# Optimization experiments

Measured on AMD Instinct MI355X. Metric: run time of the kernel, lower is better.

## Reference

```python
import jax, jax.numpy as jnp
import numpy as np

N_LAYERS = 3

def setup_inputs() -> dict:
    key = jax.random.key(0)
    ks = jax.random.split(key, 16)
    N, E, F_in, H = 50000, 800000, 5, 64
    x = jax.random.normal(ks[0], (N, F_in), dtype=jnp.float32)
    edge_index = jax.random.randint(ks[1], (2, E), 0, N, dtype=jnp.int64)
    s = lambda fan_in: 1.0 / np.sqrt(fan_in)
    return {
        "x": x,
        "edge_index": edge_index,
        "W_enc": jax.random.uniform(ks[2], (F_in, H), jnp.float32, -s(F_in), s(F_in)),
        "b_enc": jnp.zeros((H,), jnp.float32),
        "conv_W": jax.random.uniform(ks[3], (N_LAYERS, H, H), jnp.float32, -s(H), s(H)),
        "conv_b": jnp.zeros((N_LAYERS, H), jnp.float32),
        "W_d1": jax.random.uniform(ks[4], (H, H // 2), jnp.float32, -s(H), s(H)),
        "b_d1": jnp.zeros((H // 2,), jnp.float32),
        "W_d2": jax.random.uniform(ks[5], (H // 2, 1), jnp.float32, -s(H // 2), s(H // 2)),
        "b_d2": jnp.zeros((1,), jnp.float32),
        "W_i1": jax.random.uniform(ks[6], (H, H // 2), jnp.float32, -s(H), s(H)),
        "b_i1": jnp.zeros((H // 2,), jnp.float32),
        "W_i2": jax.random.uniform(ks[7], (H // 2, 1), jnp.float32, -s(H // 2), s(H // 2)),
        "b_i2": jnp.zeros((1,), jnp.float32),
    }

def reference(x, edge_index, W_enc, b_enc, conv_W, conv_b,
              W_d1, b_d1, W_d2, b_d2, W_i1, b_i1, W_i2, b_i2):
    N = x.shape[0]
    # GCN normalization with self-loops (PyG GCNConv default):
    loops = jnp.arange(N, dtype=edge_index.dtype)
    row = jnp.concatenate([edge_index[0], loops])  # source
    col = jnp.concatenate([edge_index[1], loops])  # target
    deg = jax.ops.segment_sum(jnp.ones_like(row, dtype=x.dtype), col, num_segments=N)
    dinv = jax.lax.rsqrt(deg)  # deg >= 1 due to self-loops
    norm = dinv[row] * dinv[col]  # [E + N]

    h = jax.nn.relu(x @ W_enc + b_enc)  # [N, H]
    for l in range(N_LAYERS):
        hw = h @ conv_W[l]                       # [N, H]
        msg = hw[row] * norm[:, None]            # gather + scale
        agg = jax.ops.segment_sum(msg, col, num_segments=N)  # scatter-add
        h = jax.nn.relu(agg + conv_b[l])

    demand = jax.nn.relu(h @ W_d1 + b_d1) @ W_d2 + b_d2       # [N, 1]
    inventory = jax.nn.relu(h @ W_i1 + b_i1) @ W_i2 + b_i2    # [N, 1]
    return (demand, inventory)
```

## Files before the change

kernel.cpp:

```cpp
#include <hip/hip_runtime.h>
#include <hip/hip_bf16.h>


#define HDIM 64
#define PB 128
#define NPB 256
#define NPB_SHIFT 8

__device__ inline unsigned bfpack(float lo, float hi) {
    unsigned ul = __float_as_uint(lo), uh = __float_as_uint(hi);
    ul += 0x7fffu + ((ul >> 16) & 1u);
    uh += 0x7fffu + ((uh >> 16) & 1u);
    return (ul >> 16) | (uh & 0xffff0000u);
}

__device__ inline float2 bfunpack(unsigned u) {
    float2 r;
    r.x = __uint_as_float(u << 16);
    r.y = __uint_as_float(u & 0xffff0000u);
    return r;
}

__global__ __launch_bounds__(256) void hist_pass(const int* __restrict__ dst,
                                                 unsigned* __restrict__ histT,
                                                 int E, int NB) {
    __shared__ unsigned h[256];
    int t = threadIdx.x, p = blockIdx.x;
    h[t] = 0u;
    __syncthreads();
    int chunk = (E + PB - 1) / PB;
    int lo = p * chunk, hi = min(lo + chunk, E);
    for (int e = lo + t; e < hi; e += 256)
        atomicAdd(&h[dst[e] >> NPB_SHIFT], 1u);
    __syncthreads();
    if (t < NB) histT[t * PB + p] = h[t];
}

__global__ __launch_bounds__(128) void scan_bucket(unsigned* __restrict__ histT,
                                                   unsigned* __restrict__ btot) {
    __shared__ unsigned s[PB];
    int t = threadIdx.x, k = blockIdx.x;
    unsigned v = histT[k * PB + t];
    s[t] = v;
    __syncthreads();
#pragma unroll
    for (int off = 1; off < PB; off <<= 1) {
        unsigned u = (t >= off) ? s[t - off] : 0u;
        __syncthreads();
        s[t] += u;
        __syncthreads();
    }
    histT[k * PB + t] = s[t] - v;
    if (t == PB - 1) btot[k] = s[t];
}

__global__ __launch_bounds__(256) void bin_pass(const int* __restrict__ ei,
                                                const unsigned* __restrict__ histT,
                                                const unsigned* __restrict__ btot,
                                                unsigned* __restrict__ ebuf,
                                                int E, int NB) {
    __shared__ unsigned bb[256];
    __shared__ unsigned cur[256];
    int t = threadIdx.x, p = blockIdx.x;
    unsigned bv = (t < NB) ? btot[t] : 0u;
    bb[t] = bv;
    __syncthreads();
#pragma unroll
    for (int off = 1; off < 256; off <<= 1) {
        unsigned u = (t >= off) ? bb[t - off] : 0u;
        __syncthreads();
        bb[t] += u;
        __syncthreads();
    }
    if (t < NB) cur[t] = histT[t * PB + p] + (bb[t] - bv);
    __syncthreads();
    int chunk = (E + PB - 1) / PB;
    int lo = p * chunk, hi = min(lo + chunk, E);
    for (int e = lo + t; e < hi; e += 256) {
        unsigned sN = (unsigned)ei[e];
        unsigned dN = (unsigned)ei[E + e];
        unsigned pos = atomicAdd(&cur[dN >> NPB_SHIFT], 1u);
        ebuf[pos] = ((dN & (NPB - 1u)) << 16) | sN;
    }
}

__global__ __launch_bounds__(256) void csr_pass(const unsigned* __restrict__ ebuf,
                                                const unsigned* __restrict__ btot,
                                                unsigned* __restrict__ row_ptr,
                                                float* __restrict__ dinv,
                                                int* __restrict__ csr_src,
                                                int N, int E, int NB) {
    __shared__ unsigned bb[256];
    __shared__ unsigned cntL[NPB];
    __shared__ unsigned sc[NPB];
    __shared__ unsigned cur[NPB];
    int t = threadIdx.x, k = blockIdx.x;
    unsigned bv = (t < NB) ? btot[t] : 0u;
    bb[t] = bv;
    __syncthreads();
#pragma unroll
    for (int off = 1; off < 256; off <<= 1) {
        unsigned u = (t >= off) ? bb[t - off] : 0u;
        __syncthreads();
        bb[t] += u;
        __syncthreads();
    }
    unsigned e1 = bb[k];
    unsigned e0 = e1 - btot[k];
    int nbase = k << NPB_SHIFT;
    cntL[t] = 0u;
    __syncthreads();
    for (unsigned e = e0 + t; e < e1; e += 256)
        atomicAdd(&cntL[ebuf[e] >> 16], 1u);
    __syncthreads();
    unsigned v = cntL[t];
    sc[t] = v;
    __syncthreads();
#pragma unroll
    for (int off = 1; off < NPB; off <<= 1) {
        unsigned u = (t >= off) ? sc[t - off] : 0u;
        __syncthreads();
        sc[t] += u;
        __syncthreads();
    }
    unsigned pos0 = e0 + sc[t] - v;
    cur[t] = pos0;
    int node = nbase + t;
    if (node < N) {
        row_ptr[node] = pos0;
        dinv[node] = rsqrtf((float)(v + 1u));
    }
    if (k == NB - 1 && t == 0) row_ptr[N] = (unsigned)E;
    __syncthreads();
    for (unsigned e = e0 + t; e < e1; e += 256) {
        unsigned ed = ebuf[e];
        unsigned pos = atomicAdd(&cur[ed >> 16], 1u);
        csr_src[pos] = (int)(ed & 0xffffu);
    }
}

__global__ __launch_bounds__(256) void encoder(const float* __restrict__ x,
                                               const float* __restrict__ W,
                                               const float* __restrict__ b,
                                               const float* __restrict__ dinv,
                                               unsigned* __restrict__ hn, int N) {
    int t = blockIdx.x * 256 + threadIdx.x;
    int i = t >> 5, jp = t & 31;
    if (i >= N) return;
    int j0 = 2 * jp;
    float a0 = b[j0], a1 = b[j0 + 1];
#pragma unroll
    for (int k = 0; k < 5; k++) {
        float xv = x[i * 5 + k];
        a0 = fmaf(xv, W[k * 64 + j0], a0);
        a1 = fmaf(xv, W[k * 64 + j0 + 1], a1);
    }
    float di = dinv[i];
    hn[t] = bfpack(di * fmaxf(a0, 0.0f), di * fmaxf(a1, 0.0f));
}

__global__ __launch_bounds__(256, 6) void gather4(const unsigned int* __restrict__ row_ptr,
                                                  const int* __restrict__ csr_src,
                                                  const unsigned* __restrict__ hn,
                                                  float* __restrict__ g, int N) {
    int t = blockIdx.x * 256 + threadIdx.x;
    int i = t >> 5;
    if (i >= N) return;
    int fl = t & 31;
    float2 a0 = bfunpack(hn[(size_t)i * 32 + fl]);
    float2 a1 = {0.f, 0.f}, a2 = {0.f, 0.f}, a3 = {0.f, 0.f};
    float2 a4 = {0.f, 0.f}, a5 = {0.f, 0.f}, a6 = {0.f, 0.f}, a7 = {0.f, 0.f};
    unsigned e0 = row_ptr[i];
    unsigned cnt = row_ptr[i + 1] - e0;
    const int* idx = csr_src + e0;
    unsigned u = 0;
    if (cnt >= 8) {
        int s0 = idx[0], s1 = idx[1], s2 = idx[2], s3 = idx[3];
        int s4 = idx[4], s5 = idx[5], s6 = idx[6], s7 = idx[7];
        while (true) {
            unsigned v0 = hn[(size_t)s0 * 32 + fl];
            unsigned v1 = hn[(size_t)s1 * 32 + fl];
            unsigned v2 = hn[(size_t)s2 * 32 + fl];
            unsigned v3 = hn[(size_t)s3 * 32 + fl];
            unsigned v4 = hn[(size_t)s4 * 32 + fl];
            unsigned v5 = hn[(size_t)s5 * 32 + fl];
            unsigned v6 = hn[(size_t)s6 * 32 + fl];
            unsigned v7 = hn[(size_t)s7 * 32 + fl];
            unsigned un = u + 8;
            bool more = (un + 8 <= cnt);
            if (more) {
                s0 = idx[un + 0]; s1 = idx[un + 1]; s2 = idx[un + 2]; s3 = idx[un + 3];
                s4 = idx[un + 4]; s5 = idx[un + 5]; s6 = idx[un + 6]; s7 = idx[un + 7];
            }
            float2 f0 = bfunpack(v0), f1 = bfunpack(v1), f2 = bfunpack(v2), f3 = bfunpack(v3);
            float2 f4 = bfunpack(v4), f5 = bfunpack(v5), f6 = bfunpack(v6), f7 = bfunpack(v7);
            a0.x += f0.x; a0.y += f0.y;  a1.x += f1.x; a1.y += f1.y;
            a2.x += f2.x; a2.y += f2.y;  a3.x += f3.x; a3.y += f3.y;
            a4.x += f4.x; a4.y += f4.y;  a5.x += f5.x; a5.y += f5.y;
            a6.x += f6.x; a6.y += f6.y;  a7.x += f7.x; a7.y += f7.y;
            u = un;
            if (!more) break;
        }
    }
    if (u < cnt) {
        unsigned last = cnt - 1;
        int s0 = idx[u];
        int s1 = idx[min(u + 1, last)];
        int s2 = idx[min(u + 2, last)];
        int s3 = idx[min(u + 3, last)];
        int s4 = idx[min(u + 4, last)];
        int s5 = idx[min(u + 5, last)];
        int s6 = idx[min(u + 6, last)];
        int s7 = idx[min(u + 7, last)];
        unsigned v0 = hn[(size_t)s0 * 32 + fl];
        unsigned v1 = hn[(size_t)s1 * 32 + fl];
        unsigned v2 = hn[(size_t)s2 * 32 + fl];
        unsigned v3 = hn[(size_t)s3 * 32 + fl];
        unsigned v4 = hn[(size_t)s4 * 32 + fl];
        unsigned v5 = hn[(size_t)s5 * 32 + fl];
        unsigned v6 = hn[(size_t)s6 * 32 + fl];
        unsigned v7 = hn[(size_t)s7 * 32 + fl];
        float2 f0 = bfunpack(v0), f1 = bfunpack(v1), f2 = bfunpack(v2), f3 = bfunpack(v3);
        float2 f4 = bfunpack(v4), f5 = bfunpack(v5), f6 = bfunpack(v6), f7 = bfunpack(v7);
        a0.x += f0.x;                        a0.y += f0.y;
        a1.x += (u + 1 < cnt) ? f1.x : 0.f;  a1.y += (u + 1 < cnt) ? f1.y : 0.f;
        a2.x += (u + 2 < cnt) ? f2.x : 0.f;  a2.y += (u + 2 < cnt) ? f2.y : 0.f;
        a3.x += (u + 3 < cnt) ? f3.x : 0.f;  a3.y += (u + 3 < cnt) ? f3.y : 0.f;
        a4.x += (u + 4 < cnt) ? f4.x : 0.f;  a4.y += (u + 4 < cnt) ? f4.y : 0.f;
        a5.x += (u + 5 < cnt) ? f5.x : 0.f;  a5.y += (u + 5 < cnt) ? f5.y : 0.f;
        a6.x += (u + 6 < cnt) ? f6.x : 0.f;  a6.y += (u + 6 < cnt) ? f6.y : 0.f;
        a7.x += (u + 7 < cnt) ? f7.x : 0.f;  a7.y += (u + 7 < cnt) ? f7.y : 0.f;
    }
    a0.x += a1.x; a0.y += a1.y;  a2.x += a3.x; a2.y += a3.y;
    a4.x += a5.x; a4.y += a5.y;  a6.x += a7.x; a6.y += a7.y;
    a0.x += a2.x; a0.y += a2.y;  a4.x += a6.x; a4.y += a6.y;
    a0.x += a4.x; a0.y += a4.y;
    float2* g2 = (float2*)g;
    g2[(size_t)i * 32 + fl] = a0;
}

__global__ __launch_bounds__(256) void conv_relu(const float* __restrict__ g,
                                                 const float* __restrict__ W,
                                                 const float* __restrict__ b,
                                                 const float* __restrict__ dinv,
                                                 unsigned* __restrict__ houtB,
                                                 int N) {
    __shared__ float WT[64 * 68];
    int tid = threadIdx.x;
    for (int e = tid; e < 4096; e += 256) {
        int k = e >> 6, j = e & 63;
        WT[j * 68 + k] = W[e];
    }
    __syncthreads();
    int half = tid >> 7;
    int i = blockIdx.x * 128 + (tid & 127);
    if (i >= N) return;
    float4 h[16];
    const float4* g4 = (const float4*)(g + (size_t)i * 64);
#pragma unroll
    for (int q = 0; q < 16; q++) h[q] = g4[q];
    float di = dinv[i];
    int jb = half * 32;
#pragma unroll
    for (int j0 = 0; j0 < 32; j0 += 4) {
        float4 acc = {0.f, 0.f, 0.f, 0.f};
        const float* w0 = &WT[(jb + j0) * 68];
#pragma unroll
        for (int q = 0; q < 16; q++) {
            float4 hv = h[q];
            float4 wa = *(const float4*)(w0 + 0 * 68 + 4 * q);
            float4 wb = *(const float4*)(w0 + 1 * 68 + 4 * q);
            float4 wc = *(const float4*)(w0 + 2 * 68 + 4 * q);
            float4 wd = *(const float4*)(w0 + 3 * 68 + 4 * q);
            acc.x = fmaf(hv.x, wa.x, acc.x); acc.x = fmaf(hv.y, wa.y, acc.x);
            acc.x = fmaf(hv.z, wa.z, acc.x); acc.x = fmaf(hv.w, wa.w, acc.x);
            acc.y = fmaf(hv.x, wb.x, acc.y); acc.y = fmaf(hv.y, wb.y, acc.y);
            acc.y = fmaf(hv.z, wb.z, acc.y); acc.y = fmaf(hv.w, wb.w, acc.y);
            acc.z = fmaf(hv.x, wc.x, acc.z); acc.z = fmaf(hv.y, wc.y, acc.z);
            acc.z = fmaf(hv.z, wc.z, acc.z); acc.z = fmaf(hv.w, wc.w, acc.z);
            acc.w = fmaf(hv.x, wd.x, acc.w); acc.w = fmaf(hv.y, wd.y, acc.w);
            acc.w = fmaf(hv.z, wd.z, acc.w); acc.w = fmaf(hv.w, wd.w, acc.w);
        }
        float4 y;
        y.x = fmaxf(fmaf(di, acc.x, b[jb + j0 + 0]), 0.f) * di;
        y.y = fmaxf(fmaf(di, acc.y, b[jb + j0 + 1]), 0.f) * di;
        y.z = fmaxf(fmaf(di, acc.z, b[jb + j0 + 2]), 0.f) * di;
        y.w = fmaxf(fmaf(di, acc.w, b[jb + j0 + 3]), 0.f) * di;
        uint2 p;
        p.x = bfpack(y.x, y.y);
        p.y = bfpack(y.z, y.w);
        *(uint2*)(houtB + (size_t)i * 32 + ((jb + j0) >> 1)) = p;
    }
}

__global__ __launch_bounds__(256) void conv_heads(const float* __restrict__ g,
                                                  const float* __restrict__ W,
                                                  const float* __restrict__ b,
                                                  const float* __restrict__ dinv,
                                                  const float* __restrict__ W_d1, const float* __restrict__ b_d1,
                                                  const float* __restrict__ W_d2, const float* __restrict__ b_d2,
                                                  const float* __restrict__ W_i1, const float* __restrict__ b_i1,
                                                  const float* __restrict__ W_i2, const float* __restrict__ b_i2,
                                                  float* __restrict__ out, int N) {
    __shared__ float WTa[4352];
    __shared__ float ybuf[128 * 68];
    int tid = threadIdx.x;
    for (int e = tid; e < 4096; e += 256) {
        int k = e >> 6, j = e & 63;
        WTa[j * 68 + k] = W[e];
    }
    __syncthreads();
    int half = tid >> 7;
    int n = tid & 127;
    int i = blockIdx.x * 128 + n;
    int jb = half * 32;
    if (i < N) {
        float4 h[16];
        const float4* g4 = (const float4*)(g + (size_t)i * 64);
#pragma unroll
        for (int q = 0; q < 16; q++) h[q] = g4[q];
        float di = dinv[i];
#pragma unroll
        for (int j0 = 0; j0 < 32; j0 += 4) {
            float4 acc = {0.f, 0.f, 0.f, 0.f};
            const float* w0 = &WTa[(jb + j0) * 68];
#pragma unroll
            for (int q = 0; q < 16; q++) {
                float4 hv = h[q];
                float4 wa = *(const float4*)(w0 + 0 * 68 + 4 * q);
                float4 wb = *(const float4*)(w0 + 1 * 68 + 4 * q);
                float4 wc = *(const float4*)(w0 + 2 * 68 + 4 * q);
                float4 wd = *(const float4*)(w0 + 3 * 68 + 4 * q);
                acc.x = fmaf(hv.x, wa.x, acc.x); acc.x = fmaf(hv.y, wa.y, acc.x);
                acc.x = fmaf(hv.z, wa.z, acc.x); acc.x = fmaf(hv.w, wa.w, acc.x);
                acc.y = fmaf(hv.x, wb.x, acc.y); acc.y = fmaf(hv.y, wb.y, acc.y);
                acc.y = fmaf(hv.z, wb.z, acc.y); acc.y = fmaf(hv.w, wb.w, acc.y);
                acc.z = fmaf(hv.x, wc.x, acc.z); acc.z = fmaf(hv.y, wc.y, acc.z);
                acc.z = fmaf(hv.z, wc.z, acc.z); acc.z = fmaf(hv.w, wc.w, acc.z);
                acc.w = fmaf(hv.x, wd.x, acc.w); acc.w = fmaf(hv.y, wd.y, acc.w);
                acc.w = fmaf(hv.z, wd.z, acc.w); acc.w = fmaf(hv.w, wd.w, acc.w);
            }
            float4 y;
            y.x = fmaxf(fmaf(di, acc.x, b[jb + j0 + 0]), 0.f);
            y.y = fmaxf(fmaf(di, acc.y, b[jb + j0 + 1]), 0.f);
            y.z = fmaxf(fmaf(di, acc.z, b[jb + j0 + 2]), 0.f);
            y.w = fmaxf(fmaf(di, acc.w, b[jb + j0 + 3]), 0.f);
            *(float4*)(&ybuf[n * 68 + jb + j0]) = y;
        }
    }
    __syncthreads();
    for (int e = tid; e < 2048; e += 256) {
        int k = e >> 5, j = e & 31;
        WTa[j * 68 + k] = W_d1[e];
        WTa[2176 + j * 68 + k] = W_i1[e];
    }
    __syncthreads();
    if (i >= N) return;
    float4 hr[16];
    const float4* y4 = (const float4*)(&ybuf[n * 68]);
#pragma unroll
    for (int q = 0; q < 16; q++) hr[q] = y4[q];
    int head = half;
    const float* W1T = &WTa[head * 2176];
    const float* b1 = head ? b_i1 : b_d1;
    const float* W2 = head ? W_i2 : W_d2;
    float o = head ? b_i2[0] : b_d2[0];
#pragma unroll
    for (int j0 = 0; j0 < 32; j0 += 4) {
        float4 acc = {b1[j0], b1[j0 + 1], b1[j0 + 2], b1[j0 + 3]};
        const float* w0 = &W1T[j0 * 68];
#pragma unroll
        for (int q = 0; q < 16; q++) {
            float4 hv = hr[q];
            float4 wa = *(const float4*)(w0 + 0 * 68 + 4 * q);
            float4 wb = *(const float4*)(w0 + 1 * 68 + 4 * q);
            float4 wc = *(const float4*)(w0 + 2 * 68 + 4 * q);
            float4 wd = *(const float4*)(w0 + 3 * 68 + 4 * q);
            acc.x = fmaf(hv.x, wa.x, acc.x); acc.x = fmaf(hv.y, wa.y, acc.x);
            acc.x = fmaf(hv.z, wa.z, acc.x); acc.x = fmaf(hv.w, wa.w, acc.x);
            acc.y = fmaf(hv.x, wb.x, acc.y); acc.y = fmaf(hv.y, wb.y, acc.y);
            acc.y = fmaf(hv.z, wb.z, acc.y); acc.y = fmaf(hv.w, wb.w, acc.y);
            acc.z = fmaf(hv.x, wc.x, acc.z); acc.z = fmaf(hv.y, wc.y, acc.z);
            acc.z = fmaf(hv.z, wc.z, acc.z); acc.z = fmaf(hv.w, wc.w, acc.z);
            acc.w = fmaf(hv.x, wd.x, acc.w); acc.w = fmaf(hv.y, wd.y, acc.w);
            acc.w = fmaf(hv.z, wd.z, acc.w); acc.w = fmaf(hv.w, wd.w, acc.w);
        }
        o = fmaf(fmaxf(acc.x, 0.f), W2[j0 + 0], o);
        o = fmaf(fmaxf(acc.y, 0.f), W2[j0 + 1], o);
        o = fmaf(fmaxf(acc.z, 0.f), W2[j0 + 2], o);
        o = fmaf(fmaxf(acc.w, 0.f), W2[j0 + 3], o);
    }
    out[(size_t)head * N + i] = o;
}

extern "C" void kernel_launch(void* const* d_in, const int* in_sizes, int n_in,
                              void* d_out, int out_size, void* d_ws, size_t ws_size,
                              hipStream_t stream) {
    const float* x      = (const float*)d_in[0];
    const int*   ei     = (const int*)d_in[1];
    const float* W_enc  = (const float*)d_in[2];
    const float* b_enc  = (const float*)d_in[3];
    const float* conv_W = (const float*)d_in[4];
    const float* conv_b = (const float*)d_in[5];
    const float* W_d1   = (const float*)d_in[6];
    const float* b_d1   = (const float*)d_in[7];
    const float* W_d2   = (const float*)d_in[8];
    const float* b_d2   = (const float*)d_in[9];
    const float* W_i1   = (const float*)d_in[10];
    const float* b_i1   = (const float*)d_in[11];
    const float* W_i2   = (const float*)d_in[12];
    const float* b_i2   = (const float*)d_in[13];

    const int N = in_sizes[0] / 5;
    const int E = in_sizes[1] / 2;
    const int NB = (N + NPB - 1) >> NPB_SHIFT;

    float* g    = (float*)d_ws;
    unsigned* hbf = (unsigned*)(g + (size_t)N * HDIM);
    float* dinv = (float*)(hbf + (size_t)N * 32);
    unsigned* row_ptr = (unsigned*)(dinv + N);
    unsigned* histT   = row_ptr + N + 1;
    unsigned* btot    = histT + (size_t)NB * PB;
    int* csr_src      = (int*)(btot + NB);
    unsigned* ebuf    = (unsigned*)g;
    float* out = (float*)d_out;

    const int hwBlocks = (N + 7) / 8;
    const int tnBlocks = (N + 127) / 128;

    hist_pass<<<PB, 256, 0, stream>>>(ei + E, histT, E, NB);
    scan_bucket<<<NB, 128, 0, stream>>>(histT, btot);
    bin_pass<<<PB, 256, 0, stream>>>(ei, histT, btot, ebuf, E, NB);
    csr_pass<<<NB, 256, 0, stream>>>(ebuf, btot, row_ptr, dinv, csr_src, N, E, NB);

    encoder<<<(N * 32 + 255) / 256, 256, 0, stream>>>(x, W_enc, b_enc, dinv, hbf, N);

    for (int l = 0; l < 2; l++) {
        gather4<<<hwBlocks, 256, 0, stream>>>(row_ptr, csr_src, hbf, g, N);
        conv_relu<<<tnBlocks, 256, 0, stream>>>(g, conv_W + l * HDIM * HDIM,
                                                conv_b + l * HDIM, dinv, hbf, N);
    }

    gather4<<<hwBlocks, 256, 0, stream>>>(row_ptr, csr_src, hbf, g, N);
    conv_heads<<<tnBlocks, 256, 0, stream>>>(g, conv_W + 2 * HDIM * HDIM,
                                             conv_b + 2 * HDIM, dinv,
                                             W_d1, b_d1, W_d2, b_d2,
                                             W_i1, b_i1, W_i2, b_i2, out, N);
}
```

Before: 248.4 us.

## Fuse neighbor gather with conv matmul through shared-memory staging

The separate gather and conv/heads kernels are merged into one kernel per layer. Each block gathers 64 node rows (32 lanes per row) into a transposed shared buffer, then runs the 64x64 transform with 4 threads per node, each computing 16 outputs. This removes the fp32 intermediate g round-trip through global memory and one launch per layer, and ping-pongs bf16 buffers between layers. In exchange it uses more shared memory and registers (64-float h arrays, launch bounds 4), which may lower occupancy for the latency-bound gather.

```diff
diff --git a/kernel.cpp b/kernel.cpp
--- a/kernel.cpp
+++ b/kernel.cpp
@@ -159,14 +159,10 @@
     hn[t] = bfpack(di * fmaxf(a0, 0.0f), di * fmaxf(a1, 0.0f));
 }
 
-__global__ __launch_bounds__(256, 6) void gather4(const unsigned int* __restrict__ row_ptr,
-                                                  const int* __restrict__ csr_src,
-                                                  const unsigned* __restrict__ hn,
-                                                  float* __restrict__ g, int N) {
-    int t = blockIdx.x * 256 + threadIdx.x;
-    int i = t >> 5;
-    if (i >= N) return;
-    int fl = t & 31;
+__device__ inline float2 gather_row(const unsigned* __restrict__ row_ptr,
+                                    const int* __restrict__ csr_src,
+                                    const unsigned* __restrict__ hn,
+                                    int i, int fl) {
     float2 a0 = bfunpack(hn[(size_t)i * 32 + fl]);
     float2 a1 = {0.f, 0.f}, a2 = {0.f, 0.f}, a3 = {0.f, 0.f};
     float2 a4 = {0.f, 0.f}, a5 = {0.f, 0.f}, a6 = {0.f, 0.f}, a7 = {0.f, 0.f};
@@ -235,162 +231,174 @@
     a4.x += a5.x; a4.y += a5.y;  a6.x += a7.x; a6.y += a7.y;
     a0.x += a2.x; a0.y += a2.y;  a4.x += a6.x; a4.y += a6.y;
     a0.x += a4.x; a0.y += a4.y;
-    float2* g2 = (float2*)g;
-    g2[(size_t)i * 32 + fl] = a0;
-}
-
-__global__ __launch_bounds__(256) void conv_relu(const float* __restrict__ g,
-                                                 const float* __restrict__ W,
-                                                 const float* __restrict__ b,
-                                                 const float* __restrict__ dinv,
-                                                 unsigned* __restrict__ houtB,
-                                                 int N) {
+    return a0;
+}
+
+#define CONV_Q(ACC, W0, H, Q) do {                                              \
+    float4 wa = *(const float4*)((W0) + 0 * 68 + 4 * (Q));                      \
+    float4 wb = *(const float4*)((W0) + 1 * 68 + 4 * (Q));                      \
+    float4 wc = *(const float4*)((W0) + 2 * 68 + 4 * (Q));                      \
+    float4 wd = *(const float4*)((W0) + 3 * 68 + 4 * (Q));                      \
+    ACC.x = fmaf(H[4*(Q)+0], wa.x, ACC.x); ACC.x = fmaf(H[4*(Q)+1], wa.y, ACC.x); \
+    ACC.x = fmaf(H[4*(Q)+2], wa.z, ACC.x); ACC.x = fmaf(H[4*(Q)+3], wa.w, ACC.x); \
+    ACC.y = fmaf(H[4*(Q)+0], wb.x, ACC.y); ACC.y = fmaf(H[4*(Q)+1], wb.y, ACC.y); \
+    ACC.y = fmaf(H[4*(Q)+2], wb.z, ACC.y); ACC.y = fmaf(H[4*(Q)+3], wb.w, ACC.y); \
+    ACC.z = fmaf(H[4*(Q)+0], wc.x, ACC.z); ACC.z = fmaf(H[4*(Q)+1], wc.y, ACC.z); \
+    ACC.z = fmaf(H[4*(Q)+2], wc.z, ACC.z); ACC.z = fmaf(H[4*(Q)+3], wc.w, ACC.z); \
+    ACC.w = fmaf(H[4*(Q)+0], wd.x, ACC.w); ACC.w = fmaf(H[4*(Q)+1], wd.y, ACC.w); \
+    ACC.w = fmaf(H[4*(Q)+2], wd.z, ACC.w); ACC.w = fmaf(H[4*(Q)+3], wd.w, ACC.w); \
+} while (0)
+
+__global__ __launch_bounds__(256, 4) void gconv(const unsigned* __restrict__ row_ptr,
+                                                const int* __restrict__ csr_src,
+                                                const unsigned* __restrict__ hn_in,
+                                                const float* __restrict__ W,
+                                                const float* __restrict__ b,
+                                                const float* __restrict__ dinv,
+                                                unsigned* __restrict__ hn_out, int N) {
     __shared__ float WT[64 * 68];
+    __shared__ float ybuf[64 * 65];
     int tid = threadIdx.x;
     for (int e = tid; e < 4096; e += 256) {
         int k = e >> 6, j = e & 63;
         WT[j * 68 + k] = W[e];
     }
-    __syncthreads();
-    int half = tid >> 7;
-    int i = blockIdx.x * 128 + (tid & 127);
+    int hw = tid >> 5, fl = tid & 31;
+    int base = blockIdx.x * 64;
+    for (int s = 0; s < 8; s++) {
+        int n = hw * 8 + s;
+        int i = base + n;
+        if (i < N) {
+            float2 a = gather_row(row_ptr, csr_src, hn_in, i, fl);
+            ybuf[(2 * fl) * 65 + n] = a.x;
+            ybuf[(2 * fl + 1) * 65 + n] = a.y;
+        }
+    }
+    __syncthreads();
+    int n = tid & 63, qt = tid >> 6;
+    int i = base + n;
     if (i >= N) return;
-    float4 h[16];
-    const float4* g4 = (const float4*)(g + (size_t)i * 64);
-#pragma unroll
-    for (int q = 0; q < 16; q++) h[q] = g4[q];
+    float h[64];
+#pragma unroll
+    for (int k = 0; k < 64; k++) h[k] = ybuf[k * 65 + n];
     float di = dinv[i];
-    int jb = half * 32;
-#pragma unroll
-    for (int j0 = 0; j0 < 32; j0 += 4) {
+    int jb = qt * 16;
+    unsigned pk[8];
+#pragma unroll
+    for (int j0 = 0; j0 < 16; j0 += 4) {
         float4 acc = {0.f, 0.f, 0.f, 0.f};
         const float* w0 = &WT[(jb + j0) * 68];
 #pragma unroll
-        for (int q = 0; q < 16; q++) {
-            float4 hv = h[q];
-            float4 wa = *(const float4*)(w0 + 0 * 68 + 4 * q);
-            float4 wb = *(const float4*)(w0 + 1 * 68 + 4 * q);
-            float4 wc = *(const float4*)(w0 + 2 * 68 + 4 * q);
-            float4 wd = *(const float4*)(w0 + 3 * 68 + 4 * q);
-            acc.x = fmaf(hv.x, wa.x, acc.x); acc.x = fmaf(hv.y, wa.y, acc.x);
-            acc.x = fmaf(hv.z, wa.z, acc.x); acc.x = fmaf(hv.w, wa.w, acc.x);
-            acc.y = fmaf(hv.x, wb.x, acc.y); acc.y = fmaf(hv.y, wb.y, acc.y);
-            acc.y = fmaf(hv.z, wb.z, acc.y); acc.y = fmaf(hv.w, wb.w, acc.y);
-            acc.z = fmaf(hv.x, wc.x, acc.z); acc.z = fmaf(hv.y, wc.y, acc.z);
-            acc.z = fmaf(hv.z, wc.z, acc.z); acc.z = fmaf(hv.w, wc.w, acc.z);
-            acc.w = fmaf(hv.x, wd.x, acc.w); acc.w = fmaf(hv.y, wd.y, acc.w);
-            acc.w = fmaf(hv.z, wd.z, acc.w); acc.w = fmaf(hv.w, wd.w, acc.w);
-        }
+        for (int q = 0; q < 16; q++) CONV_Q(acc, w0, h, q);
         float4 y;
         y.x = fmaxf(fmaf(di, acc.x, b[jb + j0 + 0]), 0.f) * di;
         y.y = fmaxf(fmaf(di, acc.y, b[jb + j0 + 1]), 0.f) * di;
         y.z = fmaxf(fmaf(di, acc.z, b[jb + j0 + 2]), 0.f) * di;
         y.w = fmaxf(fmaf(di, acc.w, b[jb + j0 + 3]), 0.f) * di;
-        uint2 p;
-        p.x = bfpack(y.x, y.y);
-        p.y = bfpack(y.z, y.w);
-        *(uint2*)(houtB + (size_t)i * 32 + ((jb + j0) >> 1)) = p;
-    }
-}
-
-__global__ __launch_bounds__(256) void conv_heads(const float* __restrict__ g,
-                                                  const float* __restrict__ W,
-                                                  const float* __restrict__ b,
-                                                  const float* __restrict__ dinv,
-                                                  const float* __restrict__ W_d1, const float* __restrict__ b_d1,
-                                                  const float* __restrict__ W_d2, const float* __restrict__ b_d2,
-                                                  const float* __restrict__ W_i1, const float* __restrict__ b_i1,
-                                                  const float* __restrict__ W_i2, const float* __restrict__ b_i2,
-                                                  float* __restrict__ out, int N) {
-    __shared__ float WTa[4352];
-    __shared__ float ybuf[128 * 68];
+        pk[(j0 >> 1) + 0] = bfpack(y.x, y.y);
+        pk[(j0 >> 1) + 1] = bfpack(y.z, y.w);
+    }
+    uint4* dst = (uint4*)(hn_out + (size_t)i * 32 + qt * 8);
+    dst[0] = make_uint4(pk[0], pk[1], pk[2], pk[3]);
+    dst[1] = make_uint4(pk[4], pk[5], pk[6], pk[7]);
+}
+
+__global__ __launch_bounds__(256, 4) void gconv_heads(const unsigned* __restrict__ row_ptr,
+                                                      const int* __restrict__ csr_src,
+                                                      const unsigned* __restrict__ hn_in,
+                                                      const float* __restrict__ W,
+                                                      const float* __restrict__ b,
+                                                      const float* __restrict__ dinv,
+                                                      const float* __restrict__ W_d1, const float* __restrict__ b_d1,
+                                                      const float* __restrict__ W_d2, const float* __restrict__ b_d2,
+                                                      const float* __restrict__ W_i1, const float* __restrict__ b_i1,
+                                                      const float* __restrict__ W_i2, const float* __restrict__ b_i2,
+                                                      float* __restrict__ out, int N) {
+    __shared__ float WT[64 * 68];
+    __shared__ float ybuf[64 * 65];
+    __shared__ float opart[256];
     int tid = threadIdx.x;
     for (int e = tid; e < 4096; e += 256) {
         int k = e >> 6, j = e & 63;
-        WTa[j * 68 + k] = W[e];
-    }
-    __syncthreads();
-    int half = tid >> 7;
-    int n = tid & 127;
-    int i = blockIdx.x * 128 + n;
-    int jb = half * 32;
+        WT[j * 68 + k] = W[e];
+    }
+    int hw = tid >> 5, fl = tid & 31;
+    int base = blockIdx.x * 64;
+    for (int s = 0; s < 8; s++) {
+        int n = hw * 8 + s;
+        int i = base + n;
+        if (i < N) {
+            float2 a = gather_row(row_ptr, csr_src, hn_in, i, fl);
+            ybuf[(2 * fl) * 65 + n] = a.x;
+            ybuf[(2 * fl + 1) * 65 + n] = a.y;
+        }
+    }
+    __syncthreads();
+    int n = tid & 63, qt = tid >> 6;
+    int i = base + n;
+    int jb = qt * 16;
+    float y[16];
     if (i < N) {
-        float4 h[16];
-        const float4* g4 = (const float4*)(g + (size_t)i * 64);
-#pragma unroll
-        for (int q = 0; q < 16; q++) h[q] = g4[q];
+        float h[64];
+#pragma unroll
+        for (int k = 0; k < 64; k++) h[k] = ybuf[k * 65 + n];
         float di = dinv[i];
 #pragma unroll
-        for (int j0 = 0; j0 < 32; j0 += 4) {
+        for (int j0 = 0; j0 < 16; j0 += 4) {
             float4 acc = {0.f, 0.f, 0.f, 0.f};
-            const float* w0 = &WTa[(jb + j0) * 68];
-#pragma unroll
-            for (int q = 0; q < 16; q++) {
-                float4 hv = h[q];
-                float4 wa = *(const float4*)(w0 + 0 * 68 + 4 * q);
-                float4 wb = *(const float4*)(w0 + 1 * 68 + 4 * q);
-                float4 wc = *(const float4*)(w0 + 2 * 68 + 4 * q);
-                float4 wd = *(const float4*)(w0 + 3 * 68 + 4 * q);
-                acc.x = fmaf(hv.x, wa.x, acc.x); acc.x = fmaf(hv.y, wa.y, acc.x);
-                acc.x = fmaf(hv.z, wa.z, acc.x); acc.x = fmaf(hv.w, wa.w, acc.x);
-                acc.y = fmaf(hv.x, wb.x, acc.y); acc.y = fmaf(hv.y, wb.y, acc.y);
-                acc.y = fmaf(hv.z, wb.z, acc.y); acc.y = fmaf(hv.w, wb.w, acc.y);
-                acc.z = fmaf(hv.x, wc.x, acc.z); acc.z = fmaf(hv.y, wc.y, acc.z);
-                acc.z = fmaf(hv.z, wc.z, acc.z); acc.z = fmaf(hv.w, wc.w, acc.z);
-                acc.w = fmaf(hv.x, wd.x, acc.w); acc.w = fmaf(hv.y, wd.y, acc.w);
-                acc.w = fmaf(hv.z, wd.z, acc.w); acc.w = fmaf(hv.w, wd.w, acc.w);
-            }
-            float4 y;
-            y.x = fmaxf(fmaf(di, acc.x, b[jb + j0 + 0]), 0.f);
-            y.y = fmaxf(fmaf(di, acc.y, b[jb + j0 + 1]), 0.f);
-            y.z = fmaxf(fmaf(di, acc.z, b[jb + j0 + 2]), 0.f);
-            y.w = fmaxf(fmaf(di, acc.w, b[jb + j0 + 3]), 0.f);
-            *(float4*)(&ybuf[n * 68 + jb + j0]) = y;
-        }
-    }
-    __syncthreads();
+            const float* w0 = &WT[(jb + j0) * 68];
+#pragma unroll
+            for (int q = 0; q < 16; q++) CONV_Q(acc, w0, h, q);
+            y[j0 + 0] = fmaxf(fmaf(di, acc.x, b[jb + j0 + 0]), 0.f);
+            y[j0 + 1] = fmaxf(fmaf(di, acc.y, b[jb + j0 + 1]), 0.f);
+            y[j0 + 2] = fmaxf(fmaf(di, acc.z, b[jb + j0 + 2]), 0.f);
+            y[j0 + 3] = fmaxf(fmaf(di, acc.w, b[jb + j0 + 3]), 0.f);
+        }
+    }
+    __syncthreads();
+    if (i < N) {
+#pragma unroll
+        for (int jj = 0; jj < 16; jj++) ybuf[(jb + jj) * 65 + n] = y[jj];
+    }
     for (int e = tid; e < 2048; e += 256) {
         int k = e >> 5, j = e & 31;
-        WTa[j * 68 + k] = W_d1[e];
-        WTa[2176 + j * 68 + k] = W_i1[e];
-    }
-    __syncthreads();
-    if (i >= N) return;
-    float4 hr[16];
-    const float4* y4 = (const float4*)(&ybuf[n * 68]);
-#pragma unroll
-    for (int q = 0; q < 16; q++) hr[q] = y4[q];
-    int head = half;
-    const float* W1T = &WTa[head * 2176];
-    const float* b1 = head ? b_i1 : b_d1;
-    const float* W2 = head ? W_i2 : W_d2;
-    float o = head ? b_i2[0] : b_d2[0];
-#pragma unroll
-    for (int j0 = 0; j0 < 32; j0 += 4) {
-        float4 acc = {b1[j0], b1[j0 + 1], b1[j0 + 2], b1[j0 + 3]};
-        const float* w0 = &W1T[j0 * 68];
-#pragma unroll
-        for (int q = 0; q < 16; q++) {
-            float4 hv = hr[q];
-            float4 wa = *(const float4*)(w0 + 0 * 68 + 4 * q);
-            float4 wb = *(const float4*)(w0 + 1 * 68 + 4 * q);
-            float4 wc = *(const float4*)(w0 + 2 * 68 + 4 * q);
-            float4 wd = *(const float4*)(w0 + 3 * 68 + 4 * q);
-            acc.x = fmaf(hv.x, wa.x, acc.x); acc.x = fmaf(hv.y, wa.y, acc.x);
-            acc.x = fmaf(hv.z, wa.z, acc.x); acc.x = fmaf(hv.w, wa.w, acc.x);
-            acc.y = fmaf(hv.x, wb.x, acc.y); acc.y = fmaf(hv.y, wb.y, acc.y);
-            acc.y = fmaf(hv.z, wb.z, acc.y); acc.y = fmaf(hv.w, wb.w, acc.y);
-            acc.z = fmaf(hv.x, wc.x, acc.z); acc.z = fmaf(hv.y, wc.y, acc.z);
-            acc.z = fmaf(hv.z, wc.z, acc.z); acc.z = fmaf(hv.w, wc.w, acc.z);
-            acc.w = fmaf(hv.x, wd.x, acc.w); acc.w = fmaf(hv.y, wd.y, acc.w);
-            acc.w = fmaf(hv.z, wd.z, acc.w); acc.w = fmaf(hv.w, wd.w, acc.w);
-        }
-        o = fmaf(fmaxf(acc.x, 0.f), W2[j0 + 0], o);
-        o = fmaf(fmaxf(acc.y, 0.f), W2[j0 + 1], o);
-        o = fmaf(fmaxf(acc.z, 0.f), W2[j0 + 2], o);
-        o = fmaf(fmaxf(acc.w, 0.f), W2[j0 + 3], o);
-    }
-    out[(size_t)head * N + i] = o;
+        WT[j * 68 + k] = W_d1[e];
+        WT[2176 + j * 68 + k] = W_i1[e];
+    }
+    __syncthreads();
+    int head = qt >> 1, jh = qt & 1;
+    float op = 0.f;
+    if (i < N) {
+        float hr[64];
+#pragma unroll
+        for (int k = 0; k < 64; k++) hr[k] = ybuf[k * 65 + n];
+        const float* W1T = &WT[head * 2176];
+        const float* b1 = head ? b_i1 : b_d1;
+        const float* W2 = head ? W_i2 : W_d2;
+        int hb = jh * 16;
+#pragma unroll
+        for (int j0 = 0; j0 < 16; j0 += 4) {
+            float4 acc = {b1[hb + j0 + 0], b1[hb + j0 + 1], b1[hb + j0 + 2], b1[hb + j0 + 3]};
+            const float* w0 = &W1T[(hb + j0) * 68];
+#pragma unroll
+            for (int q = 0; q < 16; q++) CONV_Q(acc, w0, hr, q);
+            op = fmaf(fmaxf(acc.x, 0.f), W2[hb + j0 + 0], op);
+            op = fmaf(fmaxf(acc.y, 0.f), W2[hb + j0 + 1], op);
+            op = fmaf(fmaxf(acc.z, 0.f), W2[hb + j0 + 2], op);
+            op = fmaf(fmaxf(acc.w, 0.f), W2[hb + j0 + 3], op);
+        }
+    }
+    opart[qt * 64 + n] = op;
+    __syncthreads();
+    if (tid < 128) {
+        int n2 = tid & 63, hd = tid >> 6;
+        int i2 = base + n2;
+        if (i2 < N) {
+            float o = opart[hd * 128 + n2] + opart[hd * 128 + 64 + n2]
+                    + (hd ? b_i2[0] : b_d2[0]);
+            out[(size_t)hd * N + i2] = o;
+        }
+    }
 }
 
 extern "C" void kernel_launch(void* const* d_in, const int* in_sizes, int n_in,
@@ -416,34 +424,33 @@
     const int NB = (N + NPB - 1) >> NPB_SHIFT;
 
     float* g    = (float*)d_ws;
-    unsigned* hbf = (unsigned*)(g + (size_t)N * HDIM);
-    float* dinv = (float*)(hbf + (size_t)N * 32);
+    unsigned* hnA = (unsigned*)d_ws;
+    unsigned* hnB = (unsigned*)(g + (size_t)N * HDIM);
+    float* dinv = (float*)(hnB + (size_t)N * 32);
     unsigned* row_ptr = (unsigned*)(dinv + N);
     unsigned* histT   = row_ptr + N + 1;
     unsigned* btot    = histT + (size_t)NB * PB;
     int* csr_src      = (int*)(btot + NB);
-    unsigned* ebuf    = (unsigned*)g;
+    unsigned* ebuf    = (unsigned*)d_ws;
     float* out = (float*)d_out;
 
-    const int hwBlocks = (N + 7) / 8;
-    const int tnBlocks = (N + 127) / 128;
+    const int gBlocks = (N + 63) / 64;
 
     hist_pass<<<PB, 256, 0, stream>>>(ei + E, histT, E, NB);
     scan_bucket<<<NB, 128, 0, stream>>>(histT, btot);
     bin_pass<<<PB, 256, 0, stream>>>(ei, histT, btot, ebuf, E, NB);
     csr_pass<<<NB, 256, 0, stream>>>(ebuf, btot, row_ptr, dinv, csr_src, N, E, NB);
 
-    encoder<<<(N * 32 + 255) / 256, 256, 0, stream>>>(x, W_enc, b_enc, dinv, hbf, N);
-
-    for (int l = 0; l < 2; l++) {
-        gather4<<<hwBlocks, 256, 0, stream>>>(row_ptr, csr_src, hbf, g, N);
-        conv_relu<<<tnBlocks, 256, 0, stream>>>(g, conv_W + l * HDIM * HDIM,
-                                                conv_b + l * HDIM, dinv, hbf, N);
-    }
-
-    gather4<<<hwBlocks, 256, 0, stream>>>(row_ptr, csr_src, hbf, g, N);
-    conv_heads<<<tnBlocks, 256, 0, stream>>>(g, conv_W + 2 * HDIM * HDIM,
-                                             conv_b + 2 * HDIM, dinv,
-                                             W_d1, b_d1, W_d2, b_d2,
+    encoder<<<(N * 32 + 255) / 256, 256, 0, stream>>>(x, W_enc, b_enc, dinv, hnA, N);
+
+    gconv<<<gBlocks, 256, 0, stream>>>(row_ptr, csr_src, hnA,
+                                       conv_W + 0 * HDIM * HDIM, conv_b + 0 * HDIM,
+                                       dinv, hnB, N);
+    gconv<<<gBlocks, 256, 0, stream>>>(row_ptr, csr_src, hnB,
+                                       conv_W + 1 * HDIM * HDIM, conv_b + 1 * HDIM,
+                                       dinv, hnA, N);
+    gconv_heads<<<gBlocks, 256, 0, stream>>>(row_ptr, csr_src, hnA,
+                                             conv_W + 2 * HDIM * HDIM, conv_b + 2 * HDIM,
+                                             dinv, W_d1, b_d1, W_d2, b_d2,
                                              W_i1, b_i1, W_i2, b_i2, out, N);
 }
```

Measured after the change: 240.3 us. 1.03x faster.
